# Performance work log

Measured on AMD Instinct MI355X. Metric: run time of the kernel, lower is better.

The kernel has to match this reference:

```python
import jax, jax.numpy as jnp
import numpy as np

N_NODES = 100000
N_EDGES = 3200000
N_FEAT = 128
N_GRAPHS = 1024
N_CLASSES = 10
K = 30  # global_sort_pool k


def setup_inputs() -> dict:
    key = jax.random.key(0)
    ks = jax.random.split(key, 20)
    p = lambda k, shape: jax.random.normal(k, shape, jnp.float32) * 0.1
    return {
        "x": jax.random.normal(ks[0], (N_NODES, N_FEAT), jnp.float32),
        "w1": p(ks[1], (N_FEAT, 32)), "b1": p(ks[2], (32,)),
        "w2": p(ks[3], (32, 32)),     "b2": p(ks[4], (32,)),
        "w3": p(ks[5], (32, 32)),     "b3": p(ks[6], (32,)),
        "w4": p(ks[7], (32, 1)),      "b4": p(ks[8], (1,)),
        "conv5_w": p(ks[9], (16, 1, 97)),  "conv5_b": p(ks[10], (16,)),
        "conv6_w": p(ks[11], (32, 16, 5)), "conv6_b": p(ks[12], (32,)),
        "fc1_w": p(ks[13], (352, 128)),    "fc1_b": p(ks[14], (128,)),
        "fc2_w": p(ks[15], (128, N_CLASSES)), "fc2_b": p(ks[16], (N_CLASSES,)),
        "edge_src": jax.random.randint(ks[17], (N_EDGES,), 0, N_NODES),
        "edge_dst": jax.random.randint(ks[18], (N_EDGES,), 0, N_NODES),
        "batch": jnp.sort(jax.random.randint(ks[19], (N_NODES,), 0, N_GRAPHS)),
        "num_graphs": N_GRAPHS,
    }


def _gcn_forward(x, w1, b1, w2, b2, w3, b3, w4, b4,
                 conv5_w, conv5_b, conv6_w, conv6_b,
                 fc1_w, fc1_b, fc2_w, fc2_b,
                 edge_src, edge_dst, batch, num_graphs):
    n = x.shape[0]
    # remove_self_loops: mask self-loop edges to weight 0 (shapes stay static)
    ew = (edge_src != edge_dst).astype(x.dtype)
    # gcn_norm with added self-loops (weight 1): deg includes self-loop
    deg = jax.ops.segment_sum(ew, edge_dst, num_segments=n) + 1.0
    dis = jax.lax.rsqrt(deg)                       # deg^{-1/2}
    enorm = dis[edge_src] * dis[edge_dst] * ew     # [E]
    snorm = (dis * dis)[:, None]                   # self-loop norm [n,1]

    def gcn_conv(h, W, b):
        h = h @ W                                   # [n, out]
        agg = jax.ops.segment_sum(h[edge_src] * enorm[:, None], edge_dst,
                                  num_segments=n) + h * snorm
        return agg + b

    x1 = jnp.tanh(gcn_conv(x,  w1, b1))   # [n,32]
    x2 = jnp.tanh(gcn_conv(x1, w2, b2))   # [n,32]
    x3 = jnp.tanh(gcn_conv(x2, w3, b3))   # [n,32]
    x4 = jnp.tanh(gcn_conv(x3, w4, b4))   # [n,1]
    xc = jnp.concatenate([x1, x2, x3, x4], axis=-1)  # [n,97]

    # global_sort_pool(k=K): per-graph sort by last channel, descending
    key_last = xc[:, -1]
    order = jnp.lexsort((-key_last, batch))          # primary: batch, secondary: desc key
    bs = batch[order]                                # sorted graph ids
    counts = jax.ops.segment_sum(jnp.ones_like(batch, jnp.int32), batch,
                                 num_segments=num_graphs)
    starts = jnp.cumsum(counts) - counts             # exclusive prefix sum
    rank = jnp.arange(n) - starts[bs]                # rank within own graph
    r = jnp.where(rank < K, rank, K)                 # overflow -> dummy slot K
    pooled = jnp.zeros((num_graphs, K + 1, 97), xc.dtype)
    pooled = pooled.at[bs, r].set(xc[order])
    pooled = pooled[:, :K, :].reshape(num_graphs, 1, K * 97)  # [B,1,2910]

    # Conv1d(1,16,97,97) + relu
    h = jax.lax.conv_general_dilated(pooled, conv5_w, (97,), 'VALID',
                                     dimension_numbers=('NCH', 'OIH', 'NCH'))
    h = jax.nn.relu(h + conv5_b[None, :, None])      # [B,16,30]
    # MaxPool1d(2,2)
    h = jax.lax.reduce_window(h, -jnp.inf, jax.lax.max,
                              (1, 1, 2), (1, 1, 2), 'VALID')  # [B,16,15]
    # Conv1d(16,32,5,1) + relu
    h = jax.lax.conv_general_dilated(h, conv6_w, (1,), 'VALID',
                                     dimension_numbers=('NCH', 'OIH', 'NCH'))
    h = jax.nn.relu(h + conv6_b[None, :, None])      # [B,32,11]
    h = h.reshape(num_graphs, -1)                    # [B,352]

    h = jax.nn.relu(h @ fc1_w + fc1_b)               # [B,128]; dropout = identity (eval)
    return jax.nn.log_softmax(h @ fc2_w + fc2_b, axis=-1)  # [B,num_classes]


def reference(x, w1, b1, w2, b2, w3, b3, w4, b4,
              conv5_w, conv5_b, conv6_w, conv6_b,
              fc1_w, fc1_b, fc2_w, fc2_b,
              edge_src, edge_dst, batch, num_graphs):
    return _gcn_forward(x, w1, b1, w2, b2, w3, b3, w4, b4,
                        conv5_w, conv5_b, conv6_w, conv6_b,
                        fc1_w, fc1_b, fc2_w, fc2_b,
                        edge_src, edge_dst, batch, num_graphs)
```

## Files before the change

kernel.cpp:

```cpp
#include <hip/hip_runtime.h>
#include <hip/hip_bf16.h>

#define N_NODES 100000
#define N_EDGES 3200000
#define NGRAPH 1024
#define KTOP 30
#define PELEM (NGRAPH * KTOP * 97)

#define NBKT 782
#define NBKT_PAD 392
#define NTILE 391
#define TILE 8192

typedef __hip_bfloat16 bf16;

__device__ __forceinline__ float u2f(unsigned short h) {
    return __uint_as_float(((unsigned int)h) << 16);
}
__device__ __forceinline__ float LD(const void* p, int i, int bf) {
    if (bf) return u2f(((const unsigned short*)p)[i]);
    return ((const float*)p)[i];
}

__global__ void k_detect(const void* w1, int* flag) {
    if (threadIdx.x == 0 && blockIdx.x == 0) {
        const unsigned short* u = (const unsigned short*)w1;
        int plausible = 0;
        for (int i = 0; i < 64; i++) {
            float a = fabsf(u2f(u[2 * i]));
            if (a == 0.f || (a >= 9.765625e-4f && a <= 2.0f)) plausible++;
        }
        *flag = (plausible >= 40) ? 1 : 0;
    }
}

__global__ __launch_bounds__(256) void k_bhist(const int* __restrict__ src,
                                               const int* __restrict__ dst,
                                               int* __restrict__ bhistT) {
    __shared__ int h[NBKT];
    int blk = blockIdx.x;
    for (int i = threadIdx.x; i < NBKT; i += 256) h[i] = 0;
    __syncthreads();
    int base = blk * TILE;
    for (int i = threadIdx.x; i < TILE; i += 256) {
        int e = base + i;
        if (e < N_EDGES) {
            int s = src[e], d = dst[e];
            if (s != d) atomicAdd(&h[d >> 7], 1);
        }
    }
    __syncthreads();
    for (int i = threadIdx.x; i < NBKT; i += 256) bhistT[i * NBKT_PAD + blk] = h[i];
}

__global__ __launch_bounds__(64) void k_bscan(int* __restrict__ bhistT,
                                              int* __restrict__ btot) {
    int b = blockIdx.x;
    int lane = threadIdx.x;
    int* row = &bhistT[b * NBKT_PAD];
    int carry = 0;
    for (int c = 0; c < NTILE; c += 64) {
        int idx = c + lane;
        int v = (idx < NTILE) ? row[idx] : 0;
        int sc = v;
#pragma unroll
        for (int off = 1; off < 64; off <<= 1) {
            int t = __shfl_up(sc, off);
            if (lane >= off) sc += t;
        }
        if (idx < NTILE) row[idx] = sc - v + carry;
        carry += __shfl(sc, 63);
    }
    if (lane == 0) btot[b] = carry;
}

__global__ void k_btscan(const int* __restrict__ btot, int* __restrict__ bstart) {
    __shared__ int sh[1024];
    int v = ((int)threadIdx.x < NBKT) ? btot[threadIdx.x] : 0;
    sh[threadIdx.x] = v;
    __syncthreads();
    for (int off = 1; off < 1024; off <<= 1) {
        int t = (threadIdx.x >= off) ? sh[threadIdx.x - off] : 0;
        __syncthreads();
        sh[threadIdx.x] += t;
        __syncthreads();
    }
    if ((int)threadIdx.x < NBKT) bstart[threadIdx.x] = sh[threadIdx.x] - v;
    if (threadIdx.x == NBKT - 1) bstart[NBKT] = sh[threadIdx.x];
}

__global__ __launch_bounds__(256) void k_bscatter(const int* __restrict__ src,
                                                  const int* __restrict__ dst,
                                                  const int* __restrict__ bhistT,
                                                  const int* __restrict__ bstart,
                                                  int2* __restrict__ ebuf) {
    __shared__ int cur[NBKT];
    int blk = blockIdx.x;
    for (int i = threadIdx.x; i < NBKT; i += 256)
        cur[i] = bstart[i] + bhistT[i * NBKT_PAD + blk];
    __syncthreads();
    int base = blk * TILE;
    for (int i = threadIdx.x; i < TILE; i += 256) {
        int e = base + i;
        if (e < N_EDGES) {
            int s = src[e], d = dst[e];
            if (s != d) {
                int p = atomicAdd(&cur[d >> 7], 1);
                ebuf[p] = make_int2(s, d);
            }
        }
    }
}

__global__ __launch_bounds__(256) void k_bcsr(const int2* __restrict__ ebuf,
                                              const int* __restrict__ bstart,
                                              int* __restrict__ rs,
                                              float* __restrict__ dis,
                                              int* __restrict__ csr) {
    __shared__ int dloc[128];
    __shared__ int sc[128];
    int b = blockIdx.x;
    int node0 = b << 7;
    int nn = N_NODES - node0; if (nn > 128) nn = 128;
    int tid = threadIdx.x;
    if (tid < 128) dloc[tid] = 0;
    __syncthreads();
    int s = bstart[b], e = bstart[b + 1];
    for (int i = s + tid; i < e; i += 256)
        atomicAdd(&dloc[ebuf[i].y - node0], 1);
    __syncthreads();
    if (tid < 128) sc[tid] = dloc[tid];
    __syncthreads();
    for (int off = 1; off < 128; off <<= 1) {
        int t = (tid >= off && tid < 128) ? sc[tid - off] : 0;
        __syncthreads();
        if (tid < 128) sc[tid] += t;
        __syncthreads();
    }
    if (tid < nn) {
        rs[node0 + tid] = s + sc[tid] - dloc[tid];
        dis[node0 + tid] = rsqrtf((float)dloc[tid] + 1.0f);
    }
    if (b == NBKT - 1 && tid == 0) rs[N_NODES] = e;
    __syncthreads();
    if (tid < 128) dloc[tid] = s + sc[tid] - dloc[tid];
    __syncthreads();
    for (int i = s + tid; i < e; i += 256) {
        int2 p = ebuf[i];
        int pos = atomicAdd(&dloc[p.y - node0], 1);
        csr[pos] = p.x;
    }
}

__global__ void k_gstart(const int* __restrict__ batch, int* __restrict__ gstart) {
    int g = blockIdx.x * 256 + threadIdx.x;
    if (g > NGRAPH) return;
    int lo = 0, hi = N_NODES;
    while (lo < hi) {
        int mid = (lo + hi) >> 1;
        if (batch[mid] < g) lo = mid + 1; else hi = mid;
    }
    gstart[g] = lo;
}

__global__ __launch_bounds__(256) void k_mm1(const void* __restrict__ x,
                                             const void* __restrict__ w,
                                             const int* __restrict__ flagp,
                                             const float* __restrict__ dis,
                                             float* __restrict__ ts) {
    __shared__ float Wl[128 * 32];
    __shared__ float Xs[32][128];
    int bf = *flagp;
    int tid = threadIdx.x;
    int nbase = blockIdx.x * 32;
    if (bf) {
        const ushort4* wv = (const ushort4*)w;
        for (int idx = tid; idx < 1024; idx += 256) {
            ushort4 h = wv[idx];
            int p = idx * 4;
            Wl[p] = u2f(h.x); Wl[p + 1] = u2f(h.y); Wl[p + 2] = u2f(h.z); Wl[p + 3] = u2f(h.w);
        }
        const ushort4* xv = (const ushort4*)x;
        for (int idx = tid; idx < 1024; idx += 256) {
            int nd = idx >> 5, q = idx & 31;
            ushort4 h = xv[(size_t)(nbase + nd) * 32 + q];
            float* d = &Xs[nd][q * 4];
            d[0] = u2f(h.x); d[1] = u2f(h.y); d[2] = u2f(h.z); d[3] = u2f(h.w);
        }
    } else {
        const float* wf = (const float*)w;
        for (int idx = tid; idx < 4096; idx += 256) Wl[idx] = wf[idx];
        const float* xf = (const float*)x;
        for (int idx = tid; idx < 4096; idx += 256)
            Xs[idx >> 7][idx & 127] = xf[(size_t)nbase * 128 + idx];
    }
    __syncthreads();
    int grp = tid >> 5, col = tid & 31;
    for (int rep = 0; rep < 4; rep++) {
        int sub = grp + 8 * rep;
        int node = nbase + sub;
        float acc = 0.f;
#pragma unroll 8
        for (int k = 0; k < 128; k++) acc += Xs[sub][k] * Wl[k * 32 + col];
        ts[node * 32 + col] = dis[node] * acc;
    }
}

__global__ __launch_bounds__(256) void k_mm32(const float* __restrict__ xin,
                                              const void* __restrict__ w,
                                              const int* __restrict__ flagp,
                                              const float* __restrict__ dis,
                                              float* __restrict__ ts) {
    __shared__ float Wl[32 * 32];
    __shared__ float Xs[32][32];
    int bf = *flagp;
    int tid = threadIdx.x;
    int nbase = blockIdx.x * 32;
    if (bf) {
        const ushort4* wv = (const ushort4*)w;
        for (int idx = tid; idx < 256; idx += 256) {
            ushort4 h = wv[idx];
            int p = idx * 4;
            Wl[p] = u2f(h.x); Wl[p + 1] = u2f(h.y); Wl[p + 2] = u2f(h.z); Wl[p + 3] = u2f(h.w);
        }
    } else {
        const float* wf = (const float*)w;
        for (int idx = tid; idx < 1024; idx += 256) Wl[idx] = wf[idx];
    }
    {
        const float4* xv = (const float4*)xin;
        int nd = tid >> 3, q = tid & 7;
        float4 v = xv[(size_t)(nbase + nd) * 8 + q];
        float* d = &Xs[nd][q * 4];
        d[0] = v.x; d[1] = v.y; d[2] = v.z; d[3] = v.w;
    }
    __syncthreads();
    int grp = tid >> 5, col = tid & 31;
    for (int rep = 0; rep < 4; rep++) {
        int sub = grp + 8 * rep;
        int node = nbase + sub;
        float acc = 0.f;
#pragma unroll
        for (int k = 0; k < 32; k++) acc += Xs[sub][k] * Wl[k * 32 + col];
        ts[node * 32 + col] = dis[node] * acc;
    }
}

__global__ __launch_bounds__(256) void k_mm_out1(const float* __restrict__ xin,
                                                 const void* __restrict__ w4,
                                                 const int* __restrict__ flagp,
                                                 const float* __restrict__ dis,
                                                 float* __restrict__ ts4) {
    int node = blockIdx.x * 8 + (threadIdx.x >> 5);
    int lane = threadIdx.x & 31;
    if (node >= N_NODES) return;
    int bf = *flagp;
    float v = xin[node * 32 + lane] * LD(w4, lane, bf);
    for (int off = 16; off; off >>= 1) v += __shfl_down(v, off, 32);
    if (lane == 0) ts4[node] = dis[node] * v;
}

__global__ __launch_bounds__(256) void k_agg32(const float4* __restrict__ ts,
                                               const int* __restrict__ rs,
                                               const int* __restrict__ csr,
                                               const float* __restrict__ dis,
                                               const void* __restrict__ b,
                                               const int* __restrict__ flagp,
                                               float4* __restrict__ out) {
    int node = blockIdx.x * 4 + (threadIdx.x >> 6);
    int lane = threadIdx.x & 63;
    int q   = lane & 7;
    int grp = lane >> 3;
    int bf = *flagp;
    int s = rs[node], e = rs[node + 1];
    float4 a0 = make_float4(0.f, 0.f, 0.f, 0.f);
    float4 a1 = a0, a2 = a0, a3 = a0;
    int i = s + grp;
    for (; i + 24 < e; i += 32) {
        int v0 = csr[i], v1 = csr[i + 8], v2 = csr[i + 16], v3 = csr[i + 24];
        float4 m0 = ts[v0 * 8 + q];
        float4 m1 = ts[v1 * 8 + q];
        float4 m2 = ts[v2 * 8 + q];
        float4 m3 = ts[v3 * 8 + q];
        a0.x += m0.x; a0.y += m0.y; a0.z += m0.z; a0.w += m0.w;
        a1.x += m1.x; a1.y += m1.y; a1.z += m1.z; a1.w += m1.w;
        a2.x += m2.x; a2.y += m2.y; a2.z += m2.z; a2.w += m2.w;
        a3.x += m3.x; a3.y += m3.y; a3.z += m3.z; a3.w += m3.w;
    }
    for (; i < e; i += 8) {
        float4 m = ts[csr[i] * 8 + q];
        a0.x += m.x; a0.y += m.y; a0.z += m.z; a0.w += m.w;
    }
    float4 acc;
    acc.x = (a0.x + a1.x) + (a2.x + a3.x);
    acc.y = (a0.y + a1.y) + (a2.y + a3.y);
    acc.z = (a0.z + a1.z) + (a2.z + a3.z);
    acc.w = (a0.w + a1.w) + (a2.w + a3.w);
#pragma unroll
    for (int off = 8; off < 64; off <<= 1) {
        acc.x += __shfl_xor(acc.x, off);
        acc.y += __shfl_xor(acc.y, off);
        acc.z += __shfl_xor(acc.z, off);
        acc.w += __shfl_xor(acc.w, off);
    }
    if (grp == 0) {
        float4 self = ts[node * 8 + q];
        float d = dis[node];
        float4 r;
        r.x = tanhf(d * (acc.x + self.x) + LD(b, q * 4 + 0, bf));
        r.y = tanhf(d * (acc.y + self.y) + LD(b, q * 4 + 1, bf));
        r.z = tanhf(d * (acc.z + self.z) + LD(b, q * 4 + 2, bf));
        r.w = tanhf(d * (acc.w + self.w) + LD(b, q * 4 + 3, bf));
        out[node * 8 + q] = r;
    }
}

__global__ __launch_bounds__(256) void k_agg1(const float* __restrict__ ts4,
                                              const int* __restrict__ rs,
                                              const int* __restrict__ csr,
                                              const float* __restrict__ dis,
                                              const void* __restrict__ b4,
                                              const int* __restrict__ flagp,
                                              float* __restrict__ x4) {
    int node = blockIdx.x * 16 + (threadIdx.x >> 4);
    int lane = threadIdx.x & 15;
    int s = rs[node], e = rs[node + 1];
    float acc = 0.f;
    for (int i = s + lane; i < e; i += 16) acc += ts4[csr[i]];
#pragma unroll
    for (int off = 1; off < 16; off <<= 1) acc += __shfl_xor(acc, off);
    if (lane == 0) {
        int bf = *flagp;
        x4[node] = tanhf(dis[node] * (acc + ts4[node]) + LD(b4, 0, bf));
    }
}

__global__ __launch_bounds__(256) void k_rank(const int* __restrict__ batch,
                                              const int* __restrict__ gstart,
                                              const float* __restrict__ x4,
                                              int* __restrict__ sel) {
    int i = blockIdx.x * 256 + threadIdx.x;
    if (i >= N_NODES) return;
    int g = batch[i];
    int s = gstart[g], e = gstart[g + 1];
    float ki = x4[i];
    int rank = 0;
    for (int j = s; j < e; j++) {
        float kj = x4[j];
        rank += (kj > ki) || (kj == ki && j < i);
    }
    if (rank < KTOP) sel[g * KTOP + rank] = i;
}

__global__ __launch_bounds__(256) void k_pool(const float* __restrict__ x1,
                                              const float* __restrict__ x2,
                                              const float* __restrict__ x3,
                                              const float* __restrict__ x4,
                                              const int* __restrict__ sel,
                                              float* __restrict__ P) {
    int idx = blockIdx.x * 256 + threadIdx.x;
    if (idx >= PELEM) return;
    int g = idx / (KTOP * 97);
    int r = idx - g * (KTOP * 97);
    int p = r / 97;
    int f = r - p * 97;
    int v = sel[g * KTOP + p];
    float val = 0.f;
    if (v >= 0) {
        if (f < 32)      val = x1[v * 32 + f];
        else if (f < 64) val = x2[v * 32 + f - 32];
        else if (f < 96) val = x3[v * 32 + f - 64];
        else             val = x4[v];
    }
    P[idx] = val;
}

__global__ __launch_bounds__(256) void k_head(
    const float* __restrict__ Pg,
    const void* __restrict__ w5, const void* __restrict__ b5,
    const void* __restrict__ w6, const void* __restrict__ b6,
    const void* __restrict__ f1w, const void* __restrict__ f1b,
    const void* __restrict__ f2w, const void* __restrict__ f2b,
    const int* __restrict__ flagp, void* __restrict__ out) {
    __shared__ float P[KTOP * 97];
    __shared__ float W5[16 * 97];
    __shared__ float W6[32 * 16 * 5];
    __shared__ float H5[16][30];
    __shared__ float M[16][15];
    __shared__ float H6[352];
    __shared__ float Rp[256];
    __shared__ float R1[128];
    __shared__ float L[10];
    __shared__ float mls;
    int g = blockIdx.x;
    int tid = threadIdx.x;
    int bf = *flagp;

    for (int i = tid; i < KTOP * 97; i += 256) P[i] = Pg[g * (KTOP * 97) + i];
    if (bf) {
        const ushort4* w5v = (const ushort4*)w5;
        for (int i = tid; i < 388; i += 256) {
            ushort4 h = w5v[i];
            int p = i * 4;
            W5[p] = u2f(h.x); W5[p + 1] = u2f(h.y); W5[p + 2] = u2f(h.z); W5[p + 3] = u2f(h.w);
        }
        const ushort4* w6v = (const ushort4*)w6;
        for (int i = tid; i < 640; i += 256) {
            ushort4 h = w6v[i];
            int p = i * 4;
            W6[p] = u2f(h.x); W6[p + 1] = u2f(h.y); W6[p + 2] = u2f(h.z); W6[p + 3] = u2f(h.w);
        }
    } else {
        for (int i = tid; i < 16 * 97; i += 256) W5[i] = ((const float*)w5)[i];
        for (int i = tid; i < 2560; i += 256) W6[i] = ((const float*)w6)[i];
    }
    __syncthreads();
    for (int idx = tid; idx < 480; idx += 256) {
        int o = idx / 30, p = idx - o * 30;
        float acc = LD(b5, o, bf);
        const float* pr = &P[p * 97];
        const float* wr = &W5[o * 97];
        for (int f = 0; f < 97; f++) acc += wr[f] * pr[f];
        H5[o][p] = fmaxf(acc, 0.f);
    }
    __syncthreads();
    for (int idx = tid; idx < 240; idx += 256) {
        int o = idx / 15, q = idx - o * 15;
        M[o][q] = fmaxf(H5[o][2 * q], H5[o][2 * q + 1]);
    }
    __syncthreads();
    for (int idx = tid; idx < 352; idx += 256) {
        int oc = idx / 11, tp = idx - oc * 11;
        float acc = LD(b6, oc, bf);
        const float* wr = &W6[oc * 80];
        for (int ic = 0; ic < 16; ic++) {
#pragma unroll
            for (int k = 0; k < 5; k++)
                acc += wr[ic * 5 + k] * M[ic][tp + k];
        }
        H6[idx] = fmaxf(acc, 0.f);
    }
    __syncthreads();
    {
        int half = tid >> 7, col = tid & 127;
        int base = half * 176;
        float a = 0.f;
        for (int i = 0; i < 176; i++) {
            int ii = base + i;
            a += H6[ii] * LD(f1w, ii * 128 + col, bf);
        }
        Rp[tid] = a;
    }
    __syncthreads();
    if (tid < 128) R1[tid] = fmaxf(LD(f1b, tid, bf) + Rp[tid] + Rp[128 + tid], 0.f);
    __syncthreads();
    if (tid < 10) {
        float acc = LD(f2b, tid, bf);
        for (int k = 0; k < 128; k++) acc += R1[k] * LD(f2w, k * 10 + tid, bf);
        L[tid] = acc;
    }
    __syncthreads();
    if (tid == 0) {
        float m = L[0];
        for (int c = 1; c < 10; c++) m = fmaxf(m, L[c]);
        float ssum = 0.f;
        for (int c = 0; c < 10; c++) ssum += expf(L[c] - m);
        mls = m + logf(ssum);
    }
    __syncthreads();
    if (tid < 10) {
        float v = L[tid] - mls;
        if (bf) ((bf16*)out)[g * 10 + tid] = __float2bfloat16(v);
        else    ((float*)out)[g * 10 + tid] = v;
    }
}

extern "C" void kernel_launch(void* const* d_in, const int* in_sizes, int n_in,
                              void* d_out, int out_size, void* d_ws, size_t ws_size,
                              hipStream_t stream) {
    const void* x   = d_in[0];
    const void* w1  = d_in[1];  const void* b1  = d_in[2];
    const void* w2  = d_in[3];  const void* b2  = d_in[4];
    const void* w3  = d_in[5];  const void* b3  = d_in[6];
    const void* w4  = d_in[7];  const void* b4  = d_in[8];
    const void* w5  = d_in[9];  const void* b5  = d_in[10];
    const void* w6  = d_in[11]; const void* b6  = d_in[12];
    const void* f1w = d_in[13]; const void* f1b = d_in[14];
    const void* f2w = d_in[15]; const void* f2b = d_in[16];
    const int* esrc  = (const int*)d_in[17];
    const int* edst  = (const int*)d_in[18];
    const int* batch = (const int*)d_in[19];

    char* w = (char*)d_ws;
    size_t off = 0;
    auto alloc = [&](size_t bytes) {
        void* p = w + off;
        off += (bytes + 255) & ~(size_t)255;
        return p;
    };
    int*   flag   = (int*)  alloc(256);
    int*   rs     = (int*)  alloc((size_t)(N_NODES + 1) * 4);
    float* dis    = (float*)alloc((size_t)N_NODES * 4);
    int*   csr    = (int*)  alloc((size_t)N_EDGES * 4);
    float* t      = (float*)alloc((size_t)N_NODES * 32 * 4);
    float* x1     = (float*)alloc((size_t)N_NODES * 32 * 4);
    float* x2     = (float*)alloc((size_t)N_NODES * 32 * 4);
    float* x3     = (float*)alloc((size_t)N_NODES * 32 * 4);
    float* x4     = (float*)alloc((size_t)N_NODES * 4);
    int*   gstart = (int*)  alloc((size_t)(NGRAPH + 1) * 4);
    int*   sel    = (int*)  alloc((size_t)NGRAPH * KTOP * 4);
    float* Pg     = (float*)alloc((size_t)PELEM * 4);
    int*   bhistT = (int*)  alloc((size_t)NBKT * NBKT_PAD * 4);
    int*   btot   = (int*)  alloc((size_t)NBKT * 4);
    int*   bstart = (int*)  alloc((size_t)(NBKT + 1) * 4);
    (void)ws_size; (void)n_in; (void)in_sizes; (void)out_size;

    int2* ebuf = (int2*)t;

    hipMemsetAsync(sel, 0xFF, (size_t)NGRAPH * KTOP * 4, stream);

    int nb   = (N_NODES + 255) / 256;
    int mb32 = N_NODES / 32;
    int ab   = N_NODES / 4;
    int a1b  = N_NODES / 16;
    int pb   = (PELEM + 255) / 256;

    k_detect<<<1, 64, 0, stream>>>(w1, flag);
    k_bhist<<<NTILE, 256, 0, stream>>>(esrc, edst, bhistT);
    k_bscan<<<NBKT, 64, 0, stream>>>(bhistT, btot);
    k_btscan<<<1, 1024, 0, stream>>>(btot, bstart);
    k_bscatter<<<NTILE, 256, 0, stream>>>(esrc, edst, bhistT, bstart, ebuf);
    k_bcsr<<<NBKT, 256, 0, stream>>>(ebuf, bstart, rs, dis, csr);
    k_gstart<<<5, 256, 0, stream>>>(batch, gstart);

    k_mm1<<<mb32, 256, 0, stream>>>(x, w1, flag, dis, t);
    k_agg32<<<ab, 256, 0, stream>>>((const float4*)t, rs, csr, dis, b1, flag, (float4*)x1);
    k_mm32<<<mb32, 256, 0, stream>>>(x1, w2, flag, dis, t);
    k_agg32<<<ab, 256, 0, stream>>>((const float4*)t, rs, csr, dis, b2, flag, (float4*)x2);
    k_mm32<<<mb32, 256, 0, stream>>>(x2, w3, flag, dis, t);
    k_agg32<<<ab, 256, 0, stream>>>((const float4*)t, rs, csr, dis, b3, flag, (float4*)x3);
    k_mm_out1<<<(N_NODES + 7) / 8, 256, 0, stream>>>(x3, w4, flag, dis, t);
    k_agg1<<<a1b, 256, 0, stream>>>(t, rs, csr, dis, b4, flag, x4);
    k_rank<<<nb, 256, 0, stream>>>(batch, gstart, x4, sel);
    k_pool<<<pb, 256, 0, stream>>>(x1, x2, x3, x4, sel, Pg);
    k_head<<<NGRAPH, 256, 0, stream>>>(Pg, w5, b5, w6, b6,
                                       f1w, f1b, f2w, f2b, flag, (void*)d_out);
}
```

Before: 611.5 us.

## Split GCN features into 8-wide planes and aggregate each plane separately

The 32-wide transformed features are now stored as four planes of 8 floats per node (each 3.2 MB), and aggregation runs one pass per plane, with blocks ordered by plane. Each pass gathers from a smaller working set that fits in cache better, and 8 lanes per node walk the edges sequentially, with no cross-lane reduction. The cost is that the CSR indices are read four times, each gather is a 32-byte row instead of a 128-byte one, and per-node parallelism drops, so high-degree nodes become longer serial loops.

```diff
diff --git a/kernel.cpp b/kernel.cpp
--- a/kernel.cpp
+++ b/kernel.cpp
@@ -11,6 +11,9 @@
 #define NBKT_PAD 392
 #define NTILE 391
 #define TILE 8192
+
+#define N8 (N_NODES * 8)
+#define PASS_BLOCKS (N_NODES / 32)
 
 typedef __hip_bfloat16 bf16;
 
@@ -167,7 +170,7 @@
                                              const void* __restrict__ w,
                                              const int* __restrict__ flagp,
                                              const float* __restrict__ dis,
-                                             float* __restrict__ ts) {
+                                             float* __restrict__ tsq) {
     __shared__ float Wl[128 * 32];
     __shared__ float Xs[32][128];
     int bf = *flagp;
@@ -196,13 +199,14 @@
     }
     __syncthreads();
     int grp = tid >> 5, col = tid & 31;
+    int plane = (col >> 3) * N8, j = col & 7;
     for (int rep = 0; rep < 4; rep++) {
         int sub = grp + 8 * rep;
         int node = nbase + sub;
         float acc = 0.f;
 #pragma unroll 8
         for (int k = 0; k < 128; k++) acc += Xs[sub][k] * Wl[k * 32 + col];
-        ts[node * 32 + col] = dis[node] * acc;
+        tsq[plane + node * 8 + j] = dis[node] * acc;
     }
 }
 
@@ -210,7 +214,7 @@
                                               const void* __restrict__ w,
                                               const int* __restrict__ flagp,
                                               const float* __restrict__ dis,
-                                              float* __restrict__ ts) {
+                                              float* __restrict__ tsq) {
     __shared__ float Wl[32 * 32];
     __shared__ float Xs[32][32];
     int bf = *flagp;
@@ -236,13 +240,14 @@
     }
     __syncthreads();
     int grp = tid >> 5, col = tid & 31;
+    int plane = (col >> 3) * N8, j = col & 7;
     for (int rep = 0; rep < 4; rep++) {
         int sub = grp + 8 * rep;
         int node = nbase + sub;
         float acc = 0.f;
 #pragma unroll
         for (int k = 0; k < 32; k++) acc += Xs[sub][k] * Wl[k * 32 + col];
-        ts[node * 32 + col] = dis[node] * acc;
+        tsq[plane + node * 8 + j] = dis[node] * acc;
     }
 }
 
@@ -260,59 +265,34 @@
     if (lane == 0) ts4[node] = dis[node] * v;
 }
 
-__global__ __launch_bounds__(256) void k_agg32(const float4* __restrict__ ts,
-                                               const int* __restrict__ rs,
-                                               const int* __restrict__ csr,
-                                               const float* __restrict__ dis,
-                                               const void* __restrict__ b,
-                                               const int* __restrict__ flagp,
-                                               float4* __restrict__ out) {
-    int node = blockIdx.x * 4 + (threadIdx.x >> 6);
-    int lane = threadIdx.x & 63;
-    int q   = lane & 7;
-    int grp = lane >> 3;
+__global__ __launch_bounds__(256) void k_aggs(const float* __restrict__ tsq,
+                                              const int* __restrict__ rs,
+                                              const int* __restrict__ csr,
+                                              const float* __restrict__ dis,
+                                              const void* __restrict__ b,
+                                              const int* __restrict__ flagp,
+                                              float* __restrict__ out) {
+    int pass = blockIdx.x / PASS_BLOCKS;
+    int nb   = blockIdx.x - pass * PASS_BLOCKS;
+    int node = nb * 32 + (threadIdx.x >> 3);
+    int feat = threadIdx.x & 7;
+    const float* tp = tsq + (size_t)pass * N8;
+    int s = rs[node], e = rs[node + 1];
+    float a0 = 0.f, a1 = 0.f, a2 = 0.f, a3 = 0.f;
+    int i = s;
+    for (; i + 3 < e; i += 4) {
+        int v0 = csr[i], v1 = csr[i + 1], v2 = csr[i + 2], v3 = csr[i + 3];
+        a0 += tp[v0 * 8 + feat];
+        a1 += tp[v1 * 8 + feat];
+        a2 += tp[v2 * 8 + feat];
+        a3 += tp[v3 * 8 + feat];
+    }
+    for (; i < e; i++) a0 += tp[csr[i] * 8 + feat];
     int bf = *flagp;
-    int s = rs[node], e = rs[node + 1];
-    float4 a0 = make_float4(0.f, 0.f, 0.f, 0.f);
-    float4 a1 = a0, a2 = a0, a3 = a0;
-    int i = s + grp;
-    for (; i + 24 < e; i += 32) {
-        int v0 = csr[i], v1 = csr[i + 8], v2 = csr[i + 16], v3 = csr[i + 24];
-        float4 m0 = ts[v0 * 8 + q];
-        float4 m1 = ts[v1 * 8 + q];
-        float4 m2 = ts[v2 * 8 + q];
-        float4 m3 = ts[v3 * 8 + q];
-        a0.x += m0.x; a0.y += m0.y; a0.z += m0.z; a0.w += m0.w;
-        a1.x += m1.x; a1.y += m1.y; a1.z += m1.z; a1.w += m1.w;
-        a2.x += m2.x; a2.y += m2.y; a2.z += m2.z; a2.w += m2.w;
-        a3.x += m3.x; a3.y += m3.y; a3.z += m3.z; a3.w += m3.w;
-    }
-    for (; i < e; i += 8) {
-        float4 m = ts[csr[i] * 8 + q];
-        a0.x += m.x; a0.y += m.y; a0.z += m.z; a0.w += m.w;
-    }
-    float4 acc;
-    acc.x = (a0.x + a1.x) + (a2.x + a3.x);
-    acc.y = (a0.y + a1.y) + (a2.y + a3.y);
-    acc.z = (a0.z + a1.z) + (a2.z + a3.z);
-    acc.w = (a0.w + a1.w) + (a2.w + a3.w);
-#pragma unroll
-    for (int off = 8; off < 64; off <<= 1) {
-        acc.x += __shfl_xor(acc.x, off);
-        acc.y += __shfl_xor(acc.y, off);
-        acc.z += __shfl_xor(acc.z, off);
-        acc.w += __shfl_xor(acc.w, off);
-    }
-    if (grp == 0) {
-        float4 self = ts[node * 8 + q];
-        float d = dis[node];
-        float4 r;
-        r.x = tanhf(d * (acc.x + self.x) + LD(b, q * 4 + 0, bf));
-        r.y = tanhf(d * (acc.y + self.y) + LD(b, q * 4 + 1, bf));
-        r.z = tanhf(d * (acc.z + self.z) + LD(b, q * 4 + 2, bf));
-        r.w = tanhf(d * (acc.w + self.w) + LD(b, q * 4 + 3, bf));
-        out[node * 8 + q] = r;
-    }
+    float self = tp[node * 8 + feat];
+    float d = dis[node];
+    float r = tanhf(d * (((a0 + a1) + (a2 + a3)) + self) + LD(b, pass * 8 + feat, bf));
+    out[node * 32 + pass * 8 + feat] = r;
 }
 
 __global__ __launch_bounds__(256) void k_agg1(const float* __restrict__ ts4,
@@ -521,9 +501,9 @@
 
     int nb   = (N_NODES + 255) / 256;
     int mb32 = N_NODES / 32;
-    int ab   = N_NODES / 4;
     int a1b  = N_NODES / 16;
     int pb   = (PELEM + 255) / 256;
+    int aggb = 4 * PASS_BLOCKS;
 
     k_detect<<<1, 64, 0, stream>>>(w1, flag);
     k_bhist<<<NTILE, 256, 0, stream>>>(esrc, edst, bhistT);
@@ -534,11 +514,11 @@
     k_gstart<<<5, 256, 0, stream>>>(batch, gstart);
 
     k_mm1<<<mb32, 256, 0, stream>>>(x, w1, flag, dis, t);
-    k_agg32<<<ab, 256, 0, stream>>>((const float4*)t, rs, csr, dis, b1, flag, (float4*)x1);
+    k_aggs<<<aggb, 256, 0, stream>>>(t, rs, csr, dis, b1, flag, x1);
     k_mm32<<<mb32, 256, 0, stream>>>(x1, w2, flag, dis, t);
-    k_agg32<<<ab, 256, 0, stream>>>((const float4*)t, rs, csr, dis, b2, flag, (float4*)x2);
+    k_aggs<<<aggb, 256, 0, stream>>>(t, rs, csr, dis, b2, flag, x2);
     k_mm32<<<mb32, 256, 0, stream>>>(x2, w3, flag, dis, t);
-    k_agg32<<<ab, 256, 0, stream>>>((const float4*)t, rs, csr, dis, b3, flag, (float4*)x3);
+    k_aggs<<<aggb, 256, 0, stream>>>(t, rs, csr, dis, b3, flag, x3);
     k_mm_out1<<<(N_NODES + 7) / 8, 256, 0, stream>>>(x3, w4, flag, dis, t);
     k_agg1<<<a1b, 256, 0, stream>>>(t, rs, csr, dis, b4, flag, x4);
     k_rank<<<nb, 256, 0, stream>>>(batch, gstart, x4, sel);
```

After: 704.9 us. 15.3% more time.
